# Optimization experiments

Measured on AMD Instinct MI355X. Metric: run time of the kernel, lower is better.

The kernel has to match this reference:

```python
import jax, jax.numpy as jnp
import numpy as np

M_USERS = 100000
N_ITEMS = 50000
NUM_NODES = M_USERS + N_ITEMS
DIM = 64
N_EDGES = 3200000
BATCH = 1024
N_NEGS = 40
REG = 1e-4
NUM_LAYERS = 2


def setup_inputs() -> dict:
    key = jax.random.key(0)
    ks = jax.random.split(key, 14)
    xav = lambda k, shp: jax.random.normal(k, shp, dtype=jnp.float32) * np.float32(np.sqrt(2.0 / (shp[0] + shp[-1])))
    return {
        "E": xav(ks[0], (NUM_NODES, DIM)),
        "E2": xav(ks[1], (NUM_NODES, DIM)),
        "W0": xav(ks[2], (DIM, DIM)),
        "b0": jnp.zeros((DIM,), jnp.float32),
        "W1": xav(ks[3], (DIM, DIM)),
        "b1": jnp.zeros((DIM,), jnp.float32),
        "attn_W": xav(ks[4], (DIM, DIM)),
        "attn_b": jnp.zeros((DIM,), jnp.float32),
        "q_W": xav(ks[5], (1, DIM)),
        "w": jax.random.normal(ks[6], (BATCH,), dtype=jnp.float32),
        "edge_index": jax.random.randint(ks[7], (2, N_EDGES), 0, NUM_NODES, dtype=jnp.int64),
        "u": jax.random.randint(ks[8], (BATCH,), 0, M_USERS, dtype=jnp.int64),
        "v": jax.random.randint(ks[9], (BATCH,), 0, NUM_NODES, dtype=jnp.int64),
        "n": jax.random.randint(ks[10], (BATCH, N_NEGS), 0, NUM_NODES, dtype=jnp.int64),
    }


def _aggregate(E, E2, W0, b0, W1, b1, attn_W, attn_b, q_W, row, col):
    # LightGCN branch: symmetric degree-normalized scatter-add, NUM_LAYERS hops
    deg = jax.ops.segment_sum(jnp.ones_like(col, dtype=E.dtype), col, num_segments=NUM_NODES)
    dinv = jnp.where(deg > 0, jax.lax.rsqrt(jnp.maximum(deg, 1e-12)), 0.0)
    norm = dinv[row] * dinv[col]  # [E]

    def conv(x):
        msg = norm[:, None] * x[row]  # [E, D]
        return jax.ops.segment_sum(msg, col, num_segments=NUM_NODES)

    acc = E
    x = E
    for _ in range(NUM_LAYERS):
        x = conv(x)
        acc = acc + x
    z_p = acc / (NUM_LAYERS + 1)

    # MLP branch (eval mode: dropout disabled)
    h = jax.nn.relu(E2 @ W0.T + b0)
    z_n = jax.nn.relu(h @ W1.T + b1)

    # attention fusion
    w_p = jnp.tanh(z_p @ attn_W.T + attn_b) @ q_W.T  # [NUM_NODES, 1]
    w_n = jnp.tanh(z_n @ attn_W.T + attn_b) @ q_W.T
    alpha = jax.nn.softmax(jnp.concatenate([w_p, w_n], axis=1), axis=1)
    return alpha[:, :1] * z_p + alpha[:, 1:] * z_n


def reference(E, E2, W0, b0, W1, b1, attn_W, attn_b, q_W, w, edge_index, u, v, n):
    row, col = edge_index[0], edge_index[1]
    Z = _aggregate(E, E2, W0, b0, W1, b1, attn_W, attn_b, q_W, row, col)
    u_ = Z[u]            # [B, D]
    v_ = Z[v]            # [B, D]
    n_ = Z[n]            # [B, K, D]
    pos = jnp.sum(u_ * v_, axis=1)                      # [B]
    neg = jnp.einsum('bd,bkd->bk', u_, n_)              # [B, K]
    coef = -0.5 * jnp.sign(w) + 1.5                     # [B]
    sbpr = jax.nn.log_sigmoid(coef[:, None] * pos[:, None] - neg)  # [B, K]
    reg_loss = jnp.sum(u_ ** 2) + jnp.sum(v_ ** 2) + jnp.sum(n_ ** 2)
    return -jnp.sum(sbpr) + REG * reg_loss
```

## Files before the change

kernel.cpp:

```cpp
#include <hip/hip_runtime.h>
#include <hip/hip_fp8.h>
#include <math.h>

#define NUM_NODES 150000
#define DIM 64
#define N_EDGES 3200000
#define BATCH 1024
#define N_NEGS 40
#define REG_COEF 1e-4f

#define BK_BITS 9
#define BK_NODES 512
#define NBK ((NUM_NODES + BK_NODES - 1) >> BK_BITS)
#define TILE 8192
#define NT ((N_EDGES + TILE - 1) / TILE)
#define HSIZE (NBK * NT)
#define SCAN_B 1024
#define NB2 ((HSIZE + SCAN_B - 1) / SCAN_B)
#define NLIST (BATCH * (N_NEGS + 2))

__global__ __launch_bounds__(256) void histo_kernel(const int* __restrict__ col,
                                                    int* __restrict__ hist) {
    __shared__ int h[NBK];
    int t = threadIdx.x;
    for (int i = t; i < NBK; i += 256) h[i] = 0;
    __syncthreads();
    int e0 = blockIdx.x * TILE;
    int e1 = e0 + TILE; if (e1 > N_EDGES) e1 = N_EDGES;
    for (int i = e0 + t; i < e1; i += 256) atomicAdd(&h[col[i] >> BK_BITS], 1);
    __syncthreads();
    for (int i = t; i < NBK; i += 256) hist[i * NT + blockIdx.x] = h[i];
}

__global__ void scan_partial_kernel(const int* __restrict__ src, int* __restrict__ partial, int n) {
    int t = threadIdx.x;
    int g = blockIdx.x * SCAN_B + t;
    int v = (g < n) ? src[g] : 0;
    for (int m = 1; m < 64; m <<= 1) v += __shfl_xor(v, m);
    __shared__ int ws[16];
    if ((t & 63) == 0) ws[t >> 6] = v;
    __syncthreads();
    if (t < 16) {
        int s = ws[t];
        for (int m = 1; m < 16; m <<= 1) s += __shfl_xor(s, m);
        if (t == 0) partial[blockIdx.x] = s;
    }
}

__global__ void scan_base_kernel(int* __restrict__ partial, int nb, int chunks) {
    int l = threadIdx.x;
    int carry = 0;
    for (int c = 0; c < chunks; c++) {
        int idx = c * 64 + l;
        int v = (idx < nb) ? partial[idx] : 0;
        int inc = v;
        for (int m = 1; m < 64; m <<= 1) {
            int t = __shfl_up(inc, m);
            if (l >= m) inc += t;
        }
        int excl = inc - v + carry;
        if (idx < nb) partial[idx] = excl;
        carry += __shfl(inc, 63);
    }
}

__global__ void scan_apply_kernel(int* __restrict__ data, const int* __restrict__ partial, int n) {
    __shared__ int lds[SCAN_B];
    int t = threadIdx.x;
    int g = blockIdx.x * SCAN_B + t;
    int v = (g < n) ? data[g] : 0;
    int val = v;
    lds[t] = val;
    __syncthreads();
    for (int o = 1; o < SCAN_B; o <<= 1) {
        int add = (t >= o) ? lds[t - o] : 0;
        __syncthreads();
        val += add;
        lds[t] = val;
        __syncthreads();
    }
    if (g < n) data[g] = partial[blockIdx.x] + val - v;
}

__global__ __launch_bounds__(256) void partition_kernel(const int* __restrict__ row,
                                                        const int* __restrict__ col,
                                                        const int* __restrict__ hist,
                                                        unsigned* __restrict__ staging) {
    __shared__ int base[NBK];
    __shared__ int cnt[NBK];
    int t = threadIdx.x;
    for (int i = t; i < NBK; i += 256) { base[i] = hist[i * NT + blockIdx.x]; cnt[i] = 0; }
    __syncthreads();
    int e0 = blockIdx.x * TILE;
    int e1 = e0 + TILE; if (e1 > N_EDGES) e1 = N_EDGES;
    for (int i = e0 + t; i < e1; i += 256) {
        int c = col[i];
        int b = c >> BK_BITS;
        int r = atomicAdd(&cnt[b], 1);
        staging[base[b] + r] = ((unsigned)(c & (BK_NODES - 1)) << 18) | (unsigned)row[i];
    }
}

__global__ __launch_bounds__(512) void fill3_kernel(const int* __restrict__ hist,
                                                    const unsigned* __restrict__ staging,
                                                    const float* __restrict__ E,
                                                    int* __restrict__ off,
                                                    float* __restrict__ dinv,
                                                    float* __restrict__ sq,
                                                    int* __restrict__ csr_row,
                                                    __hip_fp8x4_e4m3* __restrict__ xnE4) {
    __shared__ int cnt[BK_NODES];
    __shared__ int lds[BK_NODES];
    __shared__ float sdinv[BK_NODES];
    int b = blockIdx.x;
    int t = threadIdx.x;
    int node0 = b << BK_BITS;
    int bstart = hist[b * NT];
    int bend = (b + 1 < NBK) ? hist[(b + 1) * NT] : N_EDGES;
    cnt[t] = 0;
    __syncthreads();
    for (int i = bstart + t; i < bend; i += 512) atomicAdd(&cnt[staging[i] >> 18], 1);
    __syncthreads();
    int v = cnt[t];
    int val = v;
    lds[t] = val;
    __syncthreads();
    for (int o = 1; o < BK_NODES; o <<= 1) {
        int add = (t >= o) ? lds[t - o] : 0;
        __syncthreads();
        val += add;
        lds[t] = val;
        __syncthreads();
    }
    int cursor = bstart + val - v;
    int node = node0 + t;
    float dv = (v > 0) ? rsqrtf((float)v) : 0.f;
    if (node < NUM_NODES) {
        off[node] = cursor;
        dinv[node] = dv;
        sq[node] = sqrtf((float)v);
    }
    sdinv[t] = dv;
    cnt[t] = cursor;
    __syncthreads();
    for (int i = bstart + t; i < bend; i += 512) {
        unsigned s = staging[i];
        int pos = atomicAdd(&cnt[s >> 18], 1);
        csr_row[pos] = (int)(s & 0x3FFFFu);
    }
    int nvalid = NUM_NODES - node0; if (nvalid > BK_NODES) nvalid = BK_NODES;
    int groups = nvalid << 4;
    const float4* E4 = (const float4*)E + ((size_t)node0 << 4);
    __hip_fp8x4_e4m3* out4 = xnE4 + ((size_t)node0 << 4);
    for (int gi = t; gi < groups; gi += 512) {
        float4 e = E4[gi];
        float s = 16.f * sdinv[gi >> 4];
        out4[gi] = __hip_fp8x4_e4m3(make_float4(s * e.x, s * e.y, s * e.z, s * e.w));
    }
    if (b == 0 && t == 0) off[NUM_NODES] = N_EDGES;
}

__global__ void flag_kernel(const int* __restrict__ u, const int* __restrict__ v,
                            const int* __restrict__ n, char* __restrict__ flags) {
    int i = blockIdx.x * blockDim.x + threadIdx.x;
    if (i >= NLIST) return;
    int id;
    if (i < BATCH) id = u[i];
    else if (i < 2 * BATCH) id = v[i - BATCH];
    else id = n[i - 2 * BATCH];
    flags[id] = 1;
}

__global__ void compact_kernel(const char* __restrict__ flags, int* __restrict__ list,
                               int* __restrict__ count) {
    int i = blockIdx.x * blockDim.x + threadIdx.x;
    if (i < NUM_NODES && flags[i]) {
        int pos = atomicAdd(count, 1);
        list[pos] = i;
    }
}

__global__ __launch_bounds__(256) void conv1_kernel(const int* __restrict__ off,
                                                    const int* __restrict__ csr_row,
                                                    const float* __restrict__ dinv,
                                                    const __hip_fp8x4_e4m3* __restrict__ xq,
                                                    _Float16* __restrict__ yh) {
    int gid = blockIdx.x * blockDim.x + threadIdx.x;
    int grp = gid >> 4;
    int g = threadIdx.x & 15;
    if (grp >= NUM_NODES) return;
    int start = off[grp];
    int end = off[grp + 1];
    float a0 = 0.f, a1 = 0.f, a2 = 0.f, a3 = 0.f;
    int i = start;
    for (; i + 3 < end; i += 4) {
        int r0 = csr_row[i];
        int r1 = csr_row[i + 1];
        int r2 = csr_row[i + 2];
        int r3 = csr_row[i + 3];
        float4 v0 = static_cast<float4>(xq[((size_t)r0 << 4) + g]);
        float4 v1 = static_cast<float4>(xq[((size_t)r1 << 4) + g]);
        float4 v2 = static_cast<float4>(xq[((size_t)r2 << 4) + g]);
        float4 v3 = static_cast<float4>(xq[((size_t)r3 << 4) + g]);
        a0 += v0.x + v1.x + v2.x + v3.x;
        a1 += v0.y + v1.y + v2.y + v3.y;
        a2 += v0.z + v1.z + v2.z + v3.z;
        a3 += v0.w + v1.w + v2.w + v3.w;
    }
    for (; i < end; ++i) {
        int r = csr_row[i];
        float4 v = static_cast<float4>(xq[((size_t)r << 4) + g]);
        a0 += v.x; a1 += v.y; a2 += v.z; a3 += v.w;
    }
    float dv = dinv[grp];
    float s = dv * dv * (1.f / 16.f);
    union { _Float16 h[4]; short4 s4; } u;
    u.h[0] = (_Float16)(s * a0);
    u.h[1] = (_Float16)(s * a1);
    u.h[2] = (_Float16)(s * a2);
    u.h[3] = (_Float16)(s * a3);
    ((short4*)yh)[((size_t)grp << 4) + g] = u.s4;
}

__global__ __launch_bounds__(256) void conv2_kernel(const int* __restrict__ off,
                                                    const int* __restrict__ csr_row,
                                                    const float* __restrict__ dinv,
                                                    const _Float16* __restrict__ xh,
                                                    float* __restrict__ x2,
                                                    const int* __restrict__ list,
                                                    const int* __restrict__ count) {
    int gid = blockIdx.x * blockDim.x + threadIdx.x;
    int li = gid >> 4;
    int g = threadIdx.x & 15;
    if (li >= *count) return;
    int nd = list[li];
    int start = off[nd];
    int end = off[nd + 1];
    const short4* xh4 = (const short4*)xh;
    float a0 = 0.f, a1 = 0.f, a2 = 0.f, a3 = 0.f;
    int i = start;
    for (; i + 3 < end; i += 4) {
        int r0 = csr_row[i];
        int r1 = csr_row[i + 1];
        int r2 = csr_row[i + 2];
        int r3 = csr_row[i + 3];
        union { short4 s4; _Float16 h[4]; } u0, u1, u2, u3;
        u0.s4 = xh4[((size_t)r0 << 4) + g];
        u1.s4 = xh4[((size_t)r1 << 4) + g];
        u2.s4 = xh4[((size_t)r2 << 4) + g];
        u3.s4 = xh4[((size_t)r3 << 4) + g];
        a0 += (float)u0.h[0] + (float)u1.h[0] + (float)u2.h[0] + (float)u3.h[0];
        a1 += (float)u0.h[1] + (float)u1.h[1] + (float)u2.h[1] + (float)u3.h[1];
        a2 += (float)u0.h[2] + (float)u1.h[2] + (float)u2.h[2] + (float)u3.h[2];
        a3 += (float)u0.h[3] + (float)u1.h[3] + (float)u2.h[3] + (float)u3.h[3];
    }
    for (; i < end; ++i) {
        int r = csr_row[i];
        union { short4 s4; _Float16 h[4]; } u;
        u.s4 = xh4[((size_t)r << 4) + g];
        a0 += (float)u.h[0]; a1 += (float)u.h[1];
        a2 += (float)u.h[2]; a3 += (float)u.h[3];
    }
    float dv = dinv[nd];
    ((float4*)x2)[((size_t)nd << 4) + g] = make_float4(dv * a0, dv * a1, dv * a2, dv * a3);
}

__global__ __launch_bounds__(512) void fuse_kernel(
    const float* __restrict__ E, const float* __restrict__ E2,
    const float* __restrict__ W0, const float* __restrict__ b0,
    const float* __restrict__ W1, const float* __restrict__ b1,
    const float* __restrict__ AW, const float* __restrict__ ab,
    const float* __restrict__ qW,
    const _Float16* __restrict__ xn1, const float* __restrict__ sq,
    const float* x2, float* Z,
    const int* __restrict__ list, const int* __restrict__ count) {
    __shared__ __align__(16) float W0q[4096];
    __shared__ __align__(16) float W1q[4096];
    __shared__ __align__(16) float AWq[4096];
    __shared__ float bb0[64], bb1[64], bab[64], qb[64];
    __shared__ __align__(16) float xbuf[8][64];
    __shared__ __align__(16) float hbuf[8][64];
    __shared__ __align__(16) float zpb[8][64];
    __shared__ __align__(16) float znb[8][64];

    int t = threadIdx.x;
    for (int idx = t; idx < 4096; idx += 512) {
        int j = idx >> 6, k = idx & 63;
        int dst = (k >> 2) * 256 + j * 4 + (k & 3);
        W0q[dst] = W0[idx];
        W1q[dst] = W1[idx];
        AWq[dst] = AW[idx];
    }
    if (t < 64) { bb0[t] = b0[t]; bb1[t] = b1[t]; bab[t] = ab[t]; qb[t] = qW[t]; }
    __syncthreads();

    const int lane = t & 63, w = t >> 6;
    const int cnt = *count;
    for (int li = blockIdx.x * 8 + w; li < cnt; li += gridDim.x * 8) {
        int nd = list[li];
        size_t base = ((size_t)nd << 6) + lane;
        float x1v = sq[nd] * (float)xn1[base];
        float zp = (E[base] + x1v + x2[base]) * (1.f / 3.f);
        float e2v = E2[base];
        zpb[w][lane] = zp;
        xbuf[w][lane] = e2v;
        __builtin_amdgcn_wave_barrier();

        float s = bb0[lane];
#pragma unroll
        for (int k4 = 0; k4 < 16; k4++) {
            float4 wq = *(const float4*)&W0q[k4 * 256 + lane * 4];
            float4 xq = *(const float4*)&xbuf[w][k4 * 4];
            s += wq.x * xq.x + wq.y * xq.y + wq.z * xq.z + wq.w * xq.w;
        }
        float h = fmaxf(s, 0.f);
        hbuf[w][lane] = h;
        __builtin_amdgcn_wave_barrier();

        s = bb1[lane];
#pragma unroll
        for (int k4 = 0; k4 < 16; k4++) {
            float4 wq = *(const float4*)&W1q[k4 * 256 + lane * 4];
            float4 xq = *(const float4*)&hbuf[w][k4 * 4];
            s += wq.x * xq.x + wq.y * xq.y + wq.z * xq.z + wq.w * xq.w;
        }
        float zn = fmaxf(s, 0.f);
        znb[w][lane] = zn;
        __builtin_amdgcn_wave_barrier();

        float sp = bab[lane], sn = bab[lane];
#pragma unroll
        for (int k4 = 0; k4 < 16; k4++) {
            float4 wq = *(const float4*)&AWq[k4 * 256 + lane * 4];
            float4 zq = *(const float4*)&zpb[w][k4 * 4];
            float4 nq = *(const float4*)&znb[w][k4 * 4];
            sp += wq.x * zq.x + wq.y * zq.y + wq.z * zq.z + wq.w * zq.w;
            sn += wq.x * nq.x + wq.y * nq.y + wq.z * nq.z + wq.w * nq.w;
        }
        float tp = tanhf(sp) * qb[lane];
        float tn = tanhf(sn) * qb[lane];
        for (int m = 1; m < 64; m <<= 1) {
            tp += __shfl_xor(tp, m);
            tn += __shfl_xor(tn, m);
        }
        float mx = fmaxf(tp, tn);
        float ep = expf(tp - mx), en = expf(tn - mx);
        float inv = 1.f / (ep + en);
        Z[base] = (ep * zp + en * zn) * inv;
        __builtin_amdgcn_wave_barrier();
    }
}

__global__ __launch_bounds__(256) void loss_kernel(const float* __restrict__ Z,
                                                   const float* __restrict__ wv,
                                                   const int* __restrict__ u,
                                                   const int* __restrict__ v,
                                                   const int* __restrict__ n,
                                                   float* __restrict__ out) {
    int wid = (blockIdx.x * blockDim.x + threadIdx.x) >> 6;
    int lane = threadIdx.x & 63;
    if (wid >= BATCH) return;
    float uu = Z[(size_t)u[wid] * DIM + lane];
    float vv = Z[(size_t)v[wid] * DIM + lane];
    float pos = uu * vv;
    for (int m = 1; m < 64; m <<= 1) pos += __shfl_xor(pos, m);
    float reg = uu * uu + vv * vv;
    float wval = wv[wid];
    float sgn = (wval > 0.f ? 1.f : 0.f) - (wval < 0.f ? 1.f : 0.f);
    float coef = -0.5f * sgn + 1.5f;
    float cp = coef * pos;
    float sb = 0.f;
    for (int k = 0; k < N_NEGS; k++) {
        int nid = n[wid * N_NEGS + k];
        float nn = Z[(size_t)nid * DIM + lane];
        float d = uu * nn;
        for (int m = 1; m < 64; m <<= 1) d += __shfl_xor(d, m);
        reg += nn * nn;
        float x = cp - d;
        float ls = (x >= 0.f) ? -log1pf(expf(-x)) : (x - log1pf(expf(x)));
        sb += ls;
    }
    for (int m = 1; m < 64; m <<= 1) reg += __shfl_xor(reg, m);
    if (lane == 0) atomicAdd(out, -sb + REG_COEF * reg);
}

extern "C" void kernel_launch(void* const* d_in, const int* in_sizes, int n_in,
                              void* d_out, int out_size, void* d_ws, size_t ws_size,
                              hipStream_t stream) {
    const float* E  = (const float*)d_in[0];
    const float* E2 = (const float*)d_in[1];
    const float* W0 = (const float*)d_in[2];
    const float* b0 = (const float*)d_in[3];
    const float* W1 = (const float*)d_in[4];
    const float* b1 = (const float*)d_in[5];
    const float* AW = (const float*)d_in[6];
    const float* ab = (const float*)d_in[7];
    const float* qW = (const float*)d_in[8];
    const float* wv = (const float*)d_in[9];
    const int* ei   = (const int*)d_in[10];
    const int* uu   = (const int*)d_in[11];
    const int* vv   = (const int*)d_in[12];
    const int* nn   = (const int*)d_in[13];
    const int* row = ei;
    const int* col = ei + N_EDGES;

    char* ws = (char*)d_ws;
    size_t p = 0;
    auto align_up = [](size_t x) { return (x + 255) & ~(size_t)255; };
    int* off        = (int*)(ws + p); p = align_up(p + (size_t)(NUM_NODES + 1) * 4);
    float* dinv     = (float*)(ws + p); p = align_up(p + (size_t)NUM_NODES * 4);
    float* sq       = (float*)(ws + p); p = align_up(p + (size_t)NUM_NODES * 4);
    int* hist       = (int*)(ws + p); p = align_up(p + (size_t)HSIZE * 4);
    int* partial    = (int*)(ws + p); p = align_up(p + (size_t)NB2 * 4);
    int* csr_row    = (int*)(ws + p); p = align_up(p + (size_t)N_EDGES * 4);
    char* flags     = (char*)(ws + p); p = align_up(p + (size_t)NUM_NODES);
    int* list       = (int*)(ws + p); p = align_up(p + (size_t)NLIST * 4);
    int* count      = (int*)(ws + p); p = align_up(p + 4);
    __hip_fp8x4_e4m3* xnE4 = (__hip_fp8x4_e4m3*)(ws + p); p = align_up(p + (size_t)NUM_NODES * DIM);
    _Float16* xn1   = (_Float16*)(ws + p); p = align_up(p + (size_t)NUM_NODES * DIM * 2);
    float* x2f      = (float*)(ws + p); p = align_up(p + (size_t)NUM_NODES * DIM * 4);
    float* Z = x2f;
    unsigned* staging = (unsigned*)x2f;

    hipMemsetAsync(d_out, 0, sizeof(float), stream);
    hipMemsetAsync(flags, 0, (size_t)NUM_NODES, stream);
    hipMemsetAsync(count, 0, 4, stream);

    histo_kernel<<<NT, 256, 0, stream>>>(col, hist);
    scan_partial_kernel<<<NB2, SCAN_B, 0, stream>>>(hist, partial, HSIZE);
    scan_base_kernel<<<1, 64, 0, stream>>>(partial, NB2, 2);
    scan_apply_kernel<<<NB2, SCAN_B, 0, stream>>>(hist, partial, HSIZE);
    partition_kernel<<<NT, 256, 0, stream>>>(row, col, hist, staging);
    fill3_kernel<<<NBK, 512, 0, stream>>>(hist, staging, E, off, dinv, sq, csr_row, xnE4);

    flag_kernel<<<(NLIST + 255) / 256, 256, 0, stream>>>(uu, vv, nn, flags);
    compact_kernel<<<(NUM_NODES + 255) / 256, 256, 0, stream>>>(flags, list, count);

    conv1_kernel<<<(NUM_NODES * 16 + 255) / 256, 256, 0, stream>>>(off, csr_row, dinv, xnE4, xn1);
    conv2_kernel<<<(NLIST * 16 + 255) / 256, 256, 0, stream>>>(off, csr_row, dinv, xn1, x2f, list, count);

    fuse_kernel<<<1024, 512, 0, stream>>>(E, E2, W0, b0, W1, b1, AW, ab, qW,
                                          xn1, sq, x2f, Z, list, count);

    loss_kernel<<<BATCH * 64 / 256, 256, 0, stream>>>(Z, wv, uu, vv, nn, (float*)d_out);
}
```

Baseline: 311.6 us.

## Use fp16 dot2 weights in fuse kernel and prefetch next node's inputs

The fuse kernel now stores its three 64x64 weight matrices and the per-wave activation buffers in LDS as fp16, and computes the matvecs with fdot2 using two accumulators. It also software-prefetches the next node's E, E2, xn1, x2 and sq values while the current node is being processed, and adds a min-blocks hint to launch_bounds. The aim is to cut LDS footprint and bandwidth, shorten the dependent FMA chains, and hide global-load latency. The cost is reduced precision in the MLP and attention inputs, plus higher register pressure from the prefetched values.

```diff
diff --git a/kernel.cpp b/kernel.cpp
--- a/kernel.cpp
+++ b/kernel.cpp
@@ -18,6 +18,9 @@
 #define SCAN_B 1024
 #define NB2 ((HSIZE + SCAN_B - 1) / SCAN_B)
 #define NLIST (BATCH * (N_NEGS + 2))
+
+typedef _Float16 half2v __attribute__((ext_vector_type(2)));
+typedef _Float16 half4v __attribute__((ext_vector_type(4)));
 
 __global__ __launch_bounds__(256) void histo_kernel(const int* __restrict__ col,
                                                     int* __restrict__ hist) {
@@ -265,7 +268,7 @@
     ((float4*)x2)[((size_t)nd << 4) + g] = make_float4(dv * a0, dv * a1, dv * a2, dv * a3);
 }
 
-__global__ __launch_bounds__(512) void fuse_kernel(
+__global__ __launch_bounds__(512, 6) void fuse_kernel(
     const float* __restrict__ E, const float* __restrict__ E2,
     const float* __restrict__ W0, const float* __restrict__ b0,
     const float* __restrict__ W1, const float* __restrict__ b1,
@@ -274,71 +277,91 @@
     const _Float16* __restrict__ xn1, const float* __restrict__ sq,
     const float* x2, float* Z,
     const int* __restrict__ list, const int* __restrict__ count) {
-    __shared__ __align__(16) float W0q[4096];
-    __shared__ __align__(16) float W1q[4096];
-    __shared__ __align__(16) float AWq[4096];
+    __shared__ __align__(16) _Float16 W0h[4096];
+    __shared__ __align__(16) _Float16 W1h[4096];
+    __shared__ __align__(16) _Float16 AWh[4096];
     __shared__ float bb0[64], bb1[64], bab[64], qb[64];
-    __shared__ __align__(16) float xbuf[8][64];
-    __shared__ __align__(16) float hbuf[8][64];
-    __shared__ __align__(16) float zpb[8][64];
-    __shared__ __align__(16) float znb[8][64];
+    __shared__ __align__(16) _Float16 xb[8][64];
+    __shared__ __align__(16) _Float16 hb[8][64];
+    __shared__ __align__(16) _Float16 zpb[8][64];
+    __shared__ __align__(16) _Float16 znb[8][64];
 
     int t = threadIdx.x;
     for (int idx = t; idx < 4096; idx += 512) {
         int j = idx >> 6, k = idx & 63;
         int dst = (k >> 2) * 256 + j * 4 + (k & 3);
-        W0q[dst] = W0[idx];
-        W1q[dst] = W1[idx];
-        AWq[dst] = AW[idx];
+        W0h[dst] = (_Float16)W0[idx];
+        W1h[dst] = (_Float16)W1[idx];
+        AWh[dst] = (_Float16)AW[idx];
     }
     if (t < 64) { bb0[t] = b0[t]; bb1[t] = b1[t]; bab[t] = ab[t]; qb[t] = qW[t]; }
     __syncthreads();
 
     const int lane = t & 63, w = t >> 6;
     const int cnt = *count;
-    for (int li = blockIdx.x * 8 + w; li < cnt; li += gridDim.x * 8) {
-        int nd = list[li];
-        size_t base = ((size_t)nd << 6) + lane;
-        float x1v = sq[nd] * (float)xn1[base];
-        float zp = (E[base] + x1v + x2[base]) * (1.f / 3.f);
-        float e2v = E2[base];
-        zpb[w][lane] = zp;
-        xbuf[w][lane] = e2v;
+    const int stride = gridDim.x * 8;
+    int li = blockIdx.x * 8 + w;
+
+    int ndA = 0; float eA = 0.f, e2A = 0.f, x2A = 0.f, sqA = 0.f; _Float16 xnA = (_Float16)0.f;
+    if (li < cnt) {
+        ndA = list[li];
+        size_t bA = ((size_t)ndA << 6) + lane;
+        eA = E[bA]; e2A = E2[bA]; xnA = xn1[bA]; x2A = x2[bA]; sqA = sq[ndA];
+    }
+
+    for (; li < cnt; li += stride) {
+        int liB = li + stride;
+        int ndB = 0; float eB = 0.f, e2B = 0.f, x2B = 0.f, sqB = 0.f; _Float16 xnB = (_Float16)0.f;
+        if (liB < cnt) {
+            ndB = list[liB];
+            size_t bB = ((size_t)ndB << 6) + lane;
+            eB = E[bB]; e2B = E2[bB]; xnB = xn1[bB]; x2B = x2[bB]; sqB = sq[ndB];
+        }
+
+        size_t base = ((size_t)ndA << 6) + lane;
+        float x1v = sqA * (float)xnA;
+        float zp = (eA + x1v + x2A) * (1.f / 3.f);
+        zpb[w][lane] = (_Float16)zp;
+        xb[w][lane] = (_Float16)e2A;
         __builtin_amdgcn_wave_barrier();
 
-        float s = bb0[lane];
+        float s0 = bb0[lane], s1 = 0.f;
 #pragma unroll
         for (int k4 = 0; k4 < 16; k4++) {
-            float4 wq = *(const float4*)&W0q[k4 * 256 + lane * 4];
-            float4 xq = *(const float4*)&xbuf[w][k4 * 4];
-            s += wq.x * xq.x + wq.y * xq.y + wq.z * xq.z + wq.w * xq.w;
-        }
-        float h = fmaxf(s, 0.f);
-        hbuf[w][lane] = h;
+            half4v w4 = *(const half4v*)&W0h[k4 * 256 + lane * 4];
+            half4v x4 = *(const half4v*)&xb[w][k4 * 4];
+            s0 = __builtin_amdgcn_fdot2((half2v){w4.x, w4.y}, (half2v){x4.x, x4.y}, s0, false);
+            s1 = __builtin_amdgcn_fdot2((half2v){w4.z, w4.w}, (half2v){x4.z, x4.w}, s1, false);
+        }
+        float h = fmaxf(s0 + s1, 0.f);
+        hb[w][lane] = (_Float16)h;
         __builtin_amdgcn_wave_barrier();
 
-        s = bb1[lane];
+        s0 = bb1[lane]; s1 = 0.f;
 #pragma unroll
         for (int k4 = 0; k4 < 16; k4++) {
-            float4 wq = *(const float4*)&W1q[k4 * 256 + lane * 4];
-            float4 xq = *(const float4*)&hbuf[w][k4 * 4];
-            s += wq.x * xq.x + wq.y * xq.y + wq.z * xq.z + wq.w * xq.w;
-        }
-        float zn = fmaxf(s, 0.f);
-        znb[w][lane] = zn;
+            half4v w4 = *(const half4v*)&W1h[k4 * 256 + lane * 4];
+            half4v x4 = *(const half4v*)&hb[w][k4 * 4];
+            s0 = __builtin_amdgcn_fdot2((half2v){w4.x, w4.y}, (half2v){x4.x, x4.y}, s0, false);
+            s1 = __builtin_amdgcn_fdot2((half2v){w4.z, w4.w}, (half2v){x4.z, x4.w}, s1, false);
+        }
+        float zn = fmaxf(s0 + s1, 0.f);
+        znb[w][lane] = (_Float16)zn;
         __builtin_amdgcn_wave_barrier();
 
-        float sp = bab[lane], sn = bab[lane];
+        float sp0 = bab[lane], sp1 = 0.f, sn0 = 0.f, sn1 = 0.f;
 #pragma unroll
         for (int k4 = 0; k4 < 16; k4++) {
-            float4 wq = *(const float4*)&AWq[k4 * 256 + lane * 4];
-            float4 zq = *(const float4*)&zpb[w][k4 * 4];
-            float4 nq = *(const float4*)&znb[w][k4 * 4];
-            sp += wq.x * zq.x + wq.y * zq.y + wq.z * zq.z + wq.w * zq.w;
-            sn += wq.x * nq.x + wq.y * nq.y + wq.z * nq.z + wq.w * nq.w;
-        }
-        float tp = tanhf(sp) * qb[lane];
-        float tn = tanhf(sn) * qb[lane];
+            half4v w4 = *(const half4v*)&AWh[k4 * 256 + lane * 4];
+            half4v p4 = *(const half4v*)&zpb[w][k4 * 4];
+            half4v n4 = *(const half4v*)&znb[w][k4 * 4];
+            sp0 = __builtin_amdgcn_fdot2((half2v){w4.x, w4.y}, (half2v){p4.x, p4.y}, sp0, false);
+            sp1 = __builtin_amdgcn_fdot2((half2v){w4.z, w4.w}, (half2v){p4.z, p4.w}, sp1, false);
+            sn0 = __builtin_amdgcn_fdot2((half2v){w4.x, w4.y}, (half2v){n4.x, n4.y}, sn0, false);
+            sn1 = __builtin_amdgcn_fdot2((half2v){w4.z, w4.w}, (half2v){n4.z, n4.w}, sn1, false);
+        }
+        float tp = tanhf(sp0 + sp1) * qb[lane];
+        float tn = tanhf(bab[lane] + sn0 + sn1) * qb[lane];
         for (int m = 1; m < 64; m <<= 1) {
             tp += __shfl_xor(tp, m);
             tn += __shfl_xor(tn, m);
@@ -348,6 +371,8 @@
         float inv = 1.f / (ep + en);
         Z[base] = (ep * zp + en * zn) * inv;
         __builtin_amdgcn_wave_barrier();
+
+        ndA = ndB; eA = eB; e2A = e2B; xnA = xnB; x2A = x2B; sqA = sqB;
     }
 }
 
```

Result: slower. 326.3 us (+4.7%).
